# Kernel tuning notes

Hardware: AMD Instinct MI355X
Metric: run time of the kernel (lower is better)

## Reference

```python
import jax, jax.numpy as jnp
import numpy as np
from functools import partial

# norse LIFAdEx default parameters
DT = 0.001
TAU_SYN_INV = 1.0 / 5e-3   # 200.0
TAU_MEM_INV = 1.0 / 1e-2   # 100.0
TAU_ADA_INV = 2.0
ADAPT_CURRENT = 4.0
ADAPT_SPIKE = 0.02
DELTA_T = 0.5
V_LEAK = 0.0
V_TH = 1.0
V_RESET = 0.0
ALPHA = 100.0              # superspike surrogate sharpness
TAU_FILTER_INV = 223.1435511314


@jax.custom_vjp
def superspike(x):
    # forward: heaviside; backward: superspike surrogate grad
    return (x > 0).astype(x.dtype)

def _ss_fwd(x):
    return superspike(x), x

def _ss_bwd(x, g):
    return (g / (ALPHA * jnp.abs(x) + 1.0) ** 2,)

superspike.defvjp(_ss_fwd, _ss_bwd)


def lif_adex_recurrent(x, W_in, W_rec):
    """x: (T,B,F) -> spikes (T,B,H). norse lif_adex_step semantics."""
    T, B, _ = x.shape
    H = W_rec.shape[0]
    # precompute feed-forward input current for all steps: (T,B,H)
    i_in = jnp.einsum('tbf,hf->tbh', x, W_in)

    def step(carry, ic):
        z, v, i, a = carry
        dv = DT * TAU_MEM_INV * ((V_LEAK - v)
                                 + DELTA_T * jnp.exp((v - V_TH) / DELTA_T)
                                 + i - a)
        v_dec = v + dv
        i_dec = i - DT * TAU_SYN_INV * i
        a_dec = a + DT * TAU_ADA_INV * (ADAPT_CURRENT * (v - V_LEAK) - a)
        z_new = superspike(v_dec - V_TH)
        v_new = (1.0 - z_new) * v_dec + z_new * V_RESET
        i_new = i_dec + ic + z @ W_rec.T
        a_new = a_dec + z_new * ADAPT_SPIKE
        return (z_new, v_new, i_new, a_new), z_new

    z0 = jnp.zeros((B, H), x.dtype)
    init = (z0, z0, z0, z0)
    _, spikes = jax.lax.scan(step, init, i_in)
    return spikes


def exp_filter(spikes, W_out, b_out):
    """Linear readout + exponential low-pass filter over time."""
    y = jnp.einsum('tbh,oh->tbo', spikes, W_out) + b_out  # (T,B,O)
    k = DT * TAU_FILTER_INV

    def step(o_prev, y_t):
        o = o_prev + k * (y_t - o_prev)
        return o, o

    o0 = y[0]
    _, rest = jax.lax.scan(step, o0, y[1:])
    return jnp.concatenate([o0[None], rest], axis=0)


def setup_inputs() -> dict:
    key = jax.random.key(0)
    kx, k1, k2, k3, k4 = jax.random.split(key, 5)
    T, B, F, H, O = 500, 128, 128, 512, 32
    x = jax.random.normal(kx, (T, B, F), dtype=jnp.float32)
    W_in = jax.random.normal(k1, (H, F), dtype=jnp.float32) * np.sqrt(2.0 / F)
    W_rec = jax.random.normal(k2, (H, H), dtype=jnp.float32) * np.sqrt(2.0 / H)
    W_out = jax.random.normal(k3, (O, H), dtype=jnp.float32) * np.sqrt(1.0 / H)
    b_out = jax.random.normal(k4, (O,), dtype=jnp.float32) * 0.01
    return {'x': x, 'W_in': W_in, 'W_rec': W_rec, 'W_out': W_out, 'b_out': b_out}


def reference(x, W_in, W_rec, W_out, b_out):
    spikes = lif_adex_recurrent(x, W_in, W_rec)
    return exp_filter(spikes, W_out, b_out)
```

## Files before the change

### kernel.cpp

```cpp
#include <hip/hip_runtime.h>
#include <hip/hip_bf16.h>
#include <cstdint>
#include <cstddef>

#define T_STEPS 500
#define BATCH   128
#define FDIM    128
#define HDIM    512
#define ODIM    32
#define M_ROWS  (T_STEPS * BATCH)
#define ZOFF    (512u << 11)
#define ZOFFB   (512u << 10)

typedef __attribute__((ext_vector_type(8))) __bf16 bf16x8;
typedef __attribute__((ext_vector_type(4))) float  f32x4;

__device__ __forceinline__ float bfbits2f(unsigned short u) {
    union { unsigned int i; float f; } c; c.i = ((unsigned int)u) << 16; return c.f;
}
__device__ __forceinline__ float asf(unsigned int u) {
    union { unsigned int i; float f; } c; c.i = u; return c.f;
}
__device__ __forceinline__ void lds_barrier() {
    __builtin_amdgcn_sched_barrier(0);
    asm volatile("s_waitcnt lgkmcnt(0)" ::: "memory");
    __builtin_amdgcn_s_barrier();
    __builtin_amdgcn_sched_barrier(0);
}

__global__ void detect_kernel(const unsigned short* __restrict__ xw, int* __restrict__ flag) {
    __shared__ int cnt;
    if (threadIdx.x == 0) cnt = 0;
    __syncthreads();
    unsigned short w = xw[threadIdx.x * 2];
    int e = (w >> 7) & 0xFF;
    if (e >= 170) atomicAdd(&cnt, 1);
    __syncthreads();
    if (threadIdx.x == 0) *flag = (cnt >= 8) ? 1 : 0;
}

__global__ void prep_kernel(const void* __restrict__ Wrec,
                            const void* __restrict__ Wout,
                            const void* __restrict__ bout,
                            const void* __restrict__ Win,
                            const int* __restrict__ flag,
                            float* __restrict__ WrecT,
                            unsigned short* __restrict__ WrecTb,
                            float* __restrict__ WoutT,
                            float* __restrict__ WinT,
                            float* __restrict__ bout32) {
    const int fp32 = *flag;
    int idx = blockIdx.x * blockDim.x + threadIdx.x;
    if (fp32) {
        if (idx < HDIM * HDIM) {
            int h = idx / HDIM, hp = idx % HDIM;
            WrecT[hp * HDIM + h] = ((const float*)Wrec)[idx];
        }
        if (idx < HDIM) WrecT[HDIM * HDIM + idx] = 0.f;
        if (idx < HDIM * FDIM) {
            int h = idx / FDIM, f = idx % FDIM;
            WinT[f * HDIM + h] = ((const float*)Win)[idx];
        }
    } else {
        if (idx < HDIM * HDIM) {
            int h = idx / HDIM, hp = idx % HDIM;
            WrecTb[hp * HDIM + h] = ((const unsigned short*)Wrec)[idx];
        }
        if (idx < HDIM) WrecTb[HDIM * HDIM + idx] = 0;
    }
    if (idx < ODIM * HDIM) {
        int o = idx / HDIM, h = idx % HDIM;
        WoutT[h * ODIM + o] = fp32 ? ((const float*)Wout)[idx]
                                   : bfbits2f(((const unsigned short*)Wout)[idx]);
    }
    if (idx < ODIM)
        bout32[idx] = fp32 ? ((const float*)bout)[idx]
                           : bfbits2f(((const unsigned short*)bout)[idx]);
}

__global__ __launch_bounds__(256) void iin_gemm_mfma(const __hip_bfloat16* __restrict__ x,
                                                     const __hip_bfloat16* __restrict__ Win,
                                                     const int* __restrict__ flag,
                                                     float* __restrict__ iin) {
    if (*flag != 0) return;
    const int mt   = blockIdx.x;
    const int nt   = blockIdx.y;
    const int wave = threadIdx.x >> 6;
    const int lane = threadIdx.x & 63;
    const int l15  = lane & 15;
    const int quad = lane >> 4;
    const int m_base = mt * 64 + wave * 16;
    const int n_base = nt * 64;

    const __bf16* xb = reinterpret_cast<const __bf16*>(x);
    const __bf16* wb = reinterpret_cast<const __bf16*>(Win);

    f32x4 acc[4] = {{0.f,0.f,0.f,0.f},{0.f,0.f,0.f,0.f},{0.f,0.f,0.f,0.f},{0.f,0.f,0.f,0.f}};

#pragma unroll
    for (int kk = 0; kk < 4; ++kk) {
        const int k0 = kk * 32 + quad * 8;
        bf16x8 a = *reinterpret_cast<const bf16x8*>(xb + (size_t)(m_base + l15) * FDIM + k0);
#pragma unroll
        for (int nb = 0; nb < 4; ++nb) {
            bf16x8 bf = *reinterpret_cast<const bf16x8*>(wb + (size_t)(n_base + nb * 16 + l15) * FDIM + k0);
            acc[nb] = __builtin_amdgcn_mfma_f32_16x16x32_bf16(a, bf, acc[nb], 0, 0, 0);
        }
    }

#pragma unroll
    for (int nb = 0; nb < 4; ++nb)
#pragma unroll
        for (int r = 0; r < 4; ++r)
            iin[(size_t)(m_base + quad * 4 + r) * HDIM + n_base + nb * 16 + l15] = acc[nb][r];
}

__global__ __launch_bounds__(256) void iin_gemm_valu(const void* __restrict__ x,
                                                     const float* __restrict__ WinT,
                                                     const int* __restrict__ flag,
                                                     float* __restrict__ iin) {
    if (*flag != 1) return;
    const int tid = threadIdx.x;
    const int m0  = blockIdx.x * 32;
    const int tg  = tid >> 6;
    const int n0  = (tid & 63) * 8;

    __shared__ alignas(16) float xs[32][FDIM];

    for (int i = tid; i < 32 * FDIM; i += 256)
        xs[0][i] = ((const float*)x)[(size_t)m0 * FDIM + i];
    __syncthreads();

    const float4* xs4 = reinterpret_cast<const float4*>(&xs[tg * 8][0]);

    float acc[8][8];
#pragma unroll
    for (int i = 0; i < 8; ++i)
#pragma unroll
        for (int j = 0; j < 8; ++j) acc[i][j] = 0.f;

    auto ldw = [&](int k4, float (*w)[8]) {
#pragma unroll
        for (int u = 0; u < 4; ++u) {
            const float* wp = WinT + (size_t)(k4 * 4 + u) * HDIM + n0;
            float4 a = *(const float4*)(wp);
            float4 b = *(const float4*)(wp + 4);
            w[u][0] = a.x; w[u][1] = a.y; w[u][2] = a.z; w[u][3] = a.w;
            w[u][4] = b.x; w[u][5] = b.y; w[u][6] = b.z; w[u][7] = b.w;
        }
    };
    auto cmp = [&](int k4, const float (*w)[8]) {
#pragma unroll
        for (int i = 0; i < 8; ++i) {
            float4 xv = xs4[i * (FDIM / 4) + k4];
#pragma unroll
            for (int j = 0; j < 8; ++j)
                acc[i][j] += xv.x * w[0][j] + xv.y * w[1][j]
                           + xv.z * w[2][j] + xv.w * w[3][j];
        }
    };

    float wA[4][8], wB[4][8];
    ldw(0, wA);
    for (int k4 = 0; k4 < FDIM / 4; k4 += 2) {
        ldw(k4 + 1, wB);
        cmp(k4, wA);
        if (k4 + 2 < FDIM / 4) ldw(k4 + 2, wA);
        cmp(k4 + 1, wB);
    }

#pragma unroll
    for (int i = 0; i < 8; ++i) {
        float4 lo = {acc[i][0], acc[i][1], acc[i][2], acc[i][3]};
        float4 hi = {acc[i][4], acc[i][5], acc[i][6], acc[i][7]};
        float* op = iin + (size_t)(m0 + tg * 8 + i) * HDIM + n0;
        *(float4*)(op)     = lo;
        *(float4*)(op + 4) = hi;
    }
}

__global__ __launch_bounds__(1024) void scan_bf16(const float* __restrict__ iin,
                                                  const unsigned short* __restrict__ WrecTb,
                                                  const int* __restrict__ flag,
                                                  unsigned long long* __restrict__ masksG) {
    if (*flag != 0) return;
    const int b    = blockIdx.x;
    const int tid  = threadIdx.x;
    const int q    = tid & 63;
    const int pc   = tid >> 6;
    const int lane = tid & 63;
    const int wv   = tid >> 6;
    const bool st  = tid < HDIM;
    const int h    = tid;

    __shared__ unsigned long long wmask[8];
    __shared__ float4 partA[16][64];
    __shared__ float4 partB[16][64];
    __shared__ alignas(16) unsigned int slA[16][36];
    __shared__ alignas(16) unsigned int slB[16][36];
    unsigned int (*slO)[36] = slA;
    unsigned int (*slN)[36] = slB;

    float v = 0.f, cur = 0.f, a = 0.f;
    int   cnt = 0;
    const char* WQ = (const char*)WrecTb + q * 16;
    float ic_cur = st ? iin[(size_t)b * HDIM + h] : 0.f;

    for (int t = 0; t < T_STEPS; ++t) {
        float ic_next = 0.f;
        if (st && (t + 1) < T_STEPS)
            ic_next = iin[((size_t)(t + 1) * BATCH + b) * HDIM + h];

        float i_dec = 0.f; bool zk = false; unsigned long long m = 0;
        if (st) {
            float s = (0.0f - v) + 0.5f * expf((v - 1.0f) * 2.0f);
            s = s + cur;
            s = s - a;
            float v_dec = v + 0.1f * s;
            i_dec = cur - 0.2f * cur;
            float a_dec = a + 0.002f * (4.0f * v - a);
            zk = (v_dec - 1.0f) > 0.0f;
            m = __ballot(zk);
            if (lane == 0) {
                wmask[wv] = m;
                masksG[((size_t)t * BATCH + b) * 8 + wv] = m;
            }
            v = zk ? 0.0f : v_dec;
            a = zk ? (a_dec + 0.02f) : a_dec;
        }

        float rs0=0.f,rs1=0.f,rs2=0.f,rs3=0.f,rs4=0.f,rs5=0.f,rs6=0.f,rs7=0.f;
        {
            const unsigned int* sl = slO[pc];
            const int n  = (cnt + 15 - pc) >> 4;
            const int ng = (n + 3) >> 2;
            uint4 w0[4], w1[4];
            auto ldg = [&](int g, uint4* w) {
                uint4 ix = *(const uint4*)(sl + (g << 2));
                w[0] = *(const uint4*)(WQ + ix.x);
                w[1] = *(const uint4*)(WQ + ix.y);
                w[2] = *(const uint4*)(WQ + ix.z);
                w[3] = *(const uint4*)(WQ + ix.w);
            };
            auto accw = [&](const uint4* w) {
#pragma unroll
                for (int u = 0; u < 4; ++u) {
                    rs0 += asf(w[u].x << 16); rs1 += asf(w[u].x & 0xffff0000u);
                    rs2 += asf(w[u].y << 16); rs3 += asf(w[u].y & 0xffff0000u);
                    rs4 += asf(w[u].z << 16); rs5 += asf(w[u].z & 0xffff0000u);
                    rs6 += asf(w[u].w << 16); rs7 += asf(w[u].w & 0xffff0000u);
                }
            };
            int g = 0;
            if (ng > 0) ldg(0, w0);
            while (g + 2 <= ng) {
                ldg(g + 1, w1);
                accw(w0);
                if (g + 2 < ng) ldg(g + 2, w0);
                accw(w1);
                g += 2;
            }
            if (g < ng) accw(w0);
        }
        partA[pc][q] = (float4){rs0, rs1, rs2, rs3};
        partB[pc][q] = (float4){rs4, rs5, rs6, rs7};

        lds_barrier();

        int total = 0;
#pragma unroll
        for (int w = 0; w < 8; ++w) total += __popcll(wmask[w]);

        if (st) {
            float rec = 0.f;
            const int  qq = h >> 3, jj = h & 3;
            const bool hi = (h & 4) != 0;
#pragma unroll
            for (int pp = 0; pp < 16; ++pp) {
                const float* pa = (const float*)&partA[pp][qq];
                const float* pb = (const float*)&partB[pp][qq];
                rec += hi ? pb[jj] : pa[jj];
            }
            cur = (i_dec + ic_cur) + rec;

            if (zk) {
                int off = __popcll(m & ((1ull << lane) - 1ull));
#pragma unroll
                for (int w = 0; w < 8; ++w) if (w < wv) off += __popcll(wmask[w]);
                slN[off & 15][off >> 4] = (unsigned int)h << 10;
            }
        } else if (tid < HDIM + 64) {
            int s5 = (tid - HDIM) >> 2;
            int k  = (tid - HDIM) & 3;
            int ne = (total + 15 - s5) >> 4;
            int padc = (4 - (ne & 3)) & 3;
            if (k < padc) slN[s5][ne + k] = ZOFFB;
        }
        cnt = total;
        ic_cur = ic_next;

        lds_barrier();

        unsigned int (*tp)[36] = slO; slO = slN; slN = tp;
    }
}

__global__ __launch_bounds__(1024) void scan_f32(const float* __restrict__ iin,
                                                 const float* __restrict__ WrecT,
                                                 const int* __restrict__ flag,
                                                 unsigned long long* __restrict__ masksG) {
    if (*flag != 1) return;
    const int b    = blockIdx.x;
    const int tid  = threadIdx.x;
    const int lane = tid & 63;
    const int wv   = tid >> 6;
    const bool st  = tid < HDIM;
    const int h    = tid;
    const int p    = tid >> 7;
    const int q    = tid & 127;

    __shared__ alignas(16) unsigned int seg[2][8][64];
    __shared__ int scnt[2][8];
    __shared__ float4 part[2][8][128];

    if (tid < 8) scnt[1][tid] = 0;
    if (tid < 512) ((unsigned int*)seg[1])[tid] = ZOFF;
    lds_barrier();

    float v = 0.f, cur = 0.f, a = 0.f;
    const char* WQ = (const char*)WrecT + q * 16;

    for (int t = 0; t < T_STEPS; ++t) {
        const int cb = t & 1, pv = cb ^ 1;

        float ic = 0.f, i_dec = 0.f;
        if (st) {
            ic = iin[((size_t)t * BATCH + b) * HDIM + h];
            float s = (0.0f - v) + 0.5f * expf((v - 1.0f) * 2.0f);
            s = s + cur;
            s = s - a;
            float v_dec = v + 0.1f * s;
            i_dec = cur - 0.2f * cur;
            float a_dec = a + 0.002f * (4.0f * v - a);
            bool  zk = (v_dec - 1.0f) > 0.0f;
            unsigned long long m = __ballot(zk);
            int c = (int)__popcll(m);
            unsigned long long below = (1ull << lane) - 1ull;
            if (lane == 0) {
                scnt[cb][wv] = c;
                masksG[((size_t)t * BATCH + b) * 8 + wv] = m;
            }
            if (zk) {
                int off = (int)__popcll(m & below);
                seg[cb][wv][off] = (unsigned int)h << 11;
            } else {
                int pe = (c + 3) & ~3; pe = (pe < 4) ? 4 : pe;
                int ip = c + (int)__popcll(~m & below);
                if (ip < pe) seg[cb][wv][ip] = ZOFF;
            }
            v = zk ? 0.0f : v_dec;
            a = zk ? (a_dec + 0.02f) : a_dec;
        }

        {
            const int n  = scnt[pv][p];
            const int ng = (n + 3) >> 2;
            const unsigned int* sp = &seg[pv][p][0];
            float4 rs = {0.f, 0.f, 0.f, 0.f};
            float4 b0[4], b1[4];
            auto ld4 = [&](int g, float4* d) {
                uint4 i0 = *(const uint4*)(sp + (g << 2));
                d[0] = *(const float4*)(WQ + i0.x);
                d[1] = *(const float4*)(WQ + i0.y);
                d[2] = *(const float4*)(WQ + i0.z);
                d[3] = *(const float4*)(WQ + i0.w);
            };
            auto acc4 = [&](const float4* d) {
#pragma unroll
                for (int u = 0; u < 4; ++u) {
                    rs.x += d[u].x; rs.y += d[u].y; rs.z += d[u].z; rs.w += d[u].w;
                }
            };
            ld4(0, b0);
            int g = 0;
            while (g + 2 <= ng) {
                ld4(g + 1, b1);
                acc4(b0);
                if (g + 2 < ng) ld4(g + 2, b0);
                acc4(b1);
                g += 2;
            }
            if (g < ng) acc4(b0);
            part[cb][p][q] = rs;
        }

        lds_barrier();

        if (st) {
            float rec = 0.f;
#pragma unroll
            for (int pp = 0; pp < 8; ++pp)
                rec += ((const float*)&part[cb][pp][h >> 2])[h & 3];
            cur = (i_dec + ic) + rec;
        }
    }
}

__global__ __launch_bounds__(256) void y_kernel(const unsigned long long* __restrict__ masks,
                                                const float* __restrict__ WoutT,
                                                const float* __restrict__ bout,
                                                float* __restrict__ y) {
    const int tid = threadIdx.x;
    const int p   = blockIdx.x * 8 + (tid >> 5);
    const int o   = tid & 31;
    const unsigned long long* mp = masks + (size_t)p * 8;
    float acc = 0.f;
#pragma unroll
    for (int w = 0; w < 8; ++w) {
        unsigned long long m = mp[w];
        const float* Wb = WoutT + (size_t)w * 64 * ODIM + o;
        while (m) {
            int j = __builtin_ctzll(m);
            acc += Wb[j * ODIM];
            m &= m - 1;
        }
    }
    y[(size_t)p * ODIM + o] = acc + bout[o];
}

__global__ __launch_bounds__(64) void filter_kernel(const float* __restrict__ y,
                                                    const int* __restrict__ flag,
                                                    void* __restrict__ out) {
    const int p = blockIdx.x * 64 + threadIdx.x;
    const int fp32o = *flag;
    const float kf = 0.2231435511314f;
    float c0[10], c1[10];
#pragma unroll
    for (int u = 0; u < 10; ++u) c0[u] = y[(size_t)u * (BATCH * ODIM) + p];
    float o_state = 0.f;
    for (int base = 0; base < T_STEPS; base += 10) {
        if (base + 10 < T_STEPS) {
#pragma unroll
            for (int u = 0; u < 10; ++u)
                c1[u] = y[(size_t)(base + 10 + u) * (BATCH * ODIM) + p];
        }
#pragma unroll
        for (int u = 0; u < 10; ++u) {
            int t = base + u;
            float yt = c0[u];
            o_state = (t == 0) ? yt : (o_state + kf * (yt - o_state));
            size_t oi = (size_t)t * (BATCH * ODIM) + p;
            if (fp32o) ((float*)out)[oi] = o_state;
            else       ((__hip_bfloat16*)out)[oi] = __float2bfloat16(o_state);
        }
#pragma unroll
        for (int u = 0; u < 10; ++u) c0[u] = c1[u];
    }
}

extern "C" void kernel_launch(void* const* d_in, const int* in_sizes, int n_in,
                              void* d_out, int out_size, void* d_ws, size_t ws_size,
                              hipStream_t stream) {
    const void* x = d_in[0]; const void* Win = d_in[1]; const void* Wrec = d_in[2];
    const void* Wout = d_in[3]; const void* bout = d_in[4];
    for (int i = 0; i < n_in; ++i) {
        switch (in_sizes[i]) {
            case 8192000: x    = d_in[i]; break;
            case 65536:   Win  = d_in[i]; break;
            case 262144:  Wrec = d_in[i]; break;
            case 16384:   Wout = d_in[i]; break;
            case 32:      bout = d_in[i]; break;
            default: break;
        }
    }

    const size_t OFF_FLAG  = 0;
    const size_t OFF_BOUT  = 256;
    const size_t OFF_WOUTT = 512;
    const size_t OFF_WRECT = 66048;
    const size_t OFF_WINT  = 1116672;
    const size_t OFF_MASK  = 1378816;
    const size_t OFF_IIN   = 5474816;
    const size_t OFF_Y     = OFF_IIN;
    const size_t REQUIRED  = OFF_IIN + (size_t)M_ROWS * HDIM * 4;
    if (ws_size < REQUIRED) return;

    char* ws = (char*)d_ws;
    int*            flag   = (int*)(ws + OFF_FLAG);
    float*          bout32 = (float*)(ws + OFF_BOUT);
    float*          WoutT  = (float*)(ws + OFF_WOUTT);
    float*          WrecT  = (float*)(ws + OFF_WRECT);
    unsigned short* WrecTb = (unsigned short*)(ws + OFF_WRECT);
    float*          WinT   = (float*)(ws + OFF_WINT);
    unsigned long long* masks = (unsigned long long*)(ws + OFF_MASK);
    float*          iin    = (float*)(ws + OFF_IIN);
    float*          y      = (float*)(ws + OFF_Y);

    hipLaunchKernelGGL(detect_kernel, dim3(1), dim3(256), 0, stream,
                       (const unsigned short*)x, flag);
    hipLaunchKernelGGL(prep_kernel, dim3((HDIM * HDIM + 255) / 256), dim3(256), 0, stream,
                       Wrec, Wout, bout, Win, flag, WrecT, WrecTb, WoutT, WinT, bout32);
    hipLaunchKernelGGL(iin_gemm_mfma, dim3(M_ROWS / 64, HDIM / 64), dim3(256), 0, stream,
                       (const __hip_bfloat16*)x, (const __hip_bfloat16*)Win, flag, iin);
    hipLaunchKernelGGL(iin_gemm_valu, dim3(M_ROWS / 32), dim3(256), 0, stream,
                       x, WinT, flag, iin);
    hipLaunchKernelGGL(scan_bf16, dim3(BATCH), dim3(1024), 0, stream,
                       iin, WrecTb, flag, masks);
    hipLaunchKernelGGL(scan_f32, dim3(BATCH), dim3(1024), 0, stream,
                       iin, WrecT, flag, masks);
    hipLaunchKernelGGL(y_kernel, dim3(M_ROWS / 8), dim3(256), 0, stream,
                       masks, WoutT, bout32, y);
    hipLaunchKernelGGL(filter_kernel, dim3((BATCH * ODIM) / 64), dim3(64), 0, stream,
                       y, flag, d_out);
}
```

Baseline: 819.6 us.

## Split scan block into state and gather wavefronts, pipelining recurrent sum across steps

The scan kernel now gives threads 0-511 the neuron-state update and threads 512-1023 the sparse recurrent gather, so the two run concurrently within a step. Each gather thread covers 8 output columns (two float4 loads per spike) instead of 4, and it writes separate A/B partial buffers. The reduction of partials moves to the start of the next step's state update, which removes one barrier per step. The cost is more registers per gather thread and a one-step skew in bookkeeping (ic_prev/i_dec_prev) that must stay numerically equivalent.

```diff
diff --git a/kernel.cpp b/kernel.cpp
--- a/kernel.cpp
+++ b/kernel.cpp
@@ -316,31 +316,51 @@
     const int wv   = tid >> 6;
     const bool st  = tid < HDIM;
     const int h    = tid;
-    const int p    = tid >> 7;
-    const int q    = tid & 127;
 
     __shared__ alignas(16) unsigned int seg[2][8][64];
     __shared__ int scnt[2][8];
-    __shared__ float4 part[2][8][128];
+    __shared__ float4 partA[2][8][64];
+    __shared__ float4 partB[2][8][64];
 
     if (tid < 8) scnt[1][tid] = 0;
-    if (tid < 512) ((unsigned int*)seg[1])[tid] = ZOFF;
+    if (tid < 512) {
+        ((unsigned int*)seg[1])[tid] = ZOFF;
+        ((float4*)partA[1])[tid] = (float4){0.f, 0.f, 0.f, 0.f};
+        ((float4*)partB[1])[tid] = (float4){0.f, 0.f, 0.f, 0.f};
+    }
     lds_barrier();
 
-    float v = 0.f, cur = 0.f, a = 0.f;
-    const char* WQ = (const char*)WrecT + q * 16;
+    float v = 0.f, a = 0.f;
+    float i_dec_prev = 0.f;
+    float ic_prev = 0.f;
+
+    const int gt = tid - 512;
+    const int p  = (gt >> 6) & 7;
+    const int j  = gt & 63;
+    const char* WQ8 = (const char*)WrecT + j * 32;
 
     for (int t = 0; t < T_STEPS; ++t) {
         const int cb = t & 1, pv = cb ^ 1;
 
-        float ic = 0.f, i_dec = 0.f;
         if (st) {
-            ic = iin[((size_t)t * BATCH + b) * HDIM + h];
+            float rec = 0.f;
+            const int  jj = h >> 3, kk = h & 3;
+            const bool hi = (h & 4) != 0;
+#pragma unroll
+            for (int pp = 0; pp < 8; ++pp) {
+                const float* pa = (const float*)&partA[pv][pp][jj];
+                const float* pb = (const float*)&partB[pv][pp][jj];
+                rec += hi ? pb[kk] : pa[kk];
+            }
+            float cur = (i_dec_prev + ic_prev) + rec;
+
+            float ic_t = iin[((size_t)t * BATCH + b) * HDIM + h];
+
             float s = (0.0f - v) + 0.5f * expf((v - 1.0f) * 2.0f);
             s = s + cur;
             s = s - a;
             float v_dec = v + 0.1f * s;
-            i_dec = cur - 0.2f * cur;
+            i_dec_prev = cur - 0.2f * cur;
             float a_dec = a + 0.002f * (4.0f * v - a);
             bool  zk = (v_dec - 1.0f) > 0.0f;
             unsigned long long m = __ballot(zk);
@@ -360,49 +380,48 @@
             }
             v = zk ? 0.0f : v_dec;
             a = zk ? (a_dec + 0.02f) : a_dec;
-        }
-
-        {
+            ic_prev = ic_t;
+        } else {
             const int n  = scnt[pv][p];
             const int ng = (n + 3) >> 2;
             const unsigned int* sp = &seg[pv][p][0];
-            float4 rs = {0.f, 0.f, 0.f, 0.f};
-            float4 b0[4], b1[4];
-            auto ld4 = [&](int g, float4* d) {
-                uint4 i0 = *(const uint4*)(sp + (g << 2));
-                d[0] = *(const float4*)(WQ + i0.x);
-                d[1] = *(const float4*)(WQ + i0.y);
-                d[2] = *(const float4*)(WQ + i0.z);
-                d[3] = *(const float4*)(WQ + i0.w);
+            float rs0=0.f,rs1=0.f,rs2=0.f,rs3=0.f,rs4=0.f,rs5=0.f,rs6=0.f,rs7=0.f;
+            float4 w0[8], w1[8];
+            auto ldg = [&](int g, float4* w) {
+                uint4 ix = *(const uint4*)(sp + (g << 2));
+                w[0] = *(const float4*)(WQ8 + ix.x);
+                w[1] = *(const float4*)(WQ8 + ix.x + 16);
+                w[2] = *(const float4*)(WQ8 + ix.y);
+                w[3] = *(const float4*)(WQ8 + ix.y + 16);
+                w[4] = *(const float4*)(WQ8 + ix.z);
+                w[5] = *(const float4*)(WQ8 + ix.z + 16);
+                w[6] = *(const float4*)(WQ8 + ix.w);
+                w[7] = *(const float4*)(WQ8 + ix.w + 16);
             };
-            auto acc4 = [&](const float4* d) {
+            auto accw = [&](const float4* w) {
 #pragma unroll
                 for (int u = 0; u < 4; ++u) {
-                    rs.x += d[u].x; rs.y += d[u].y; rs.z += d[u].z; rs.w += d[u].w;
+                    rs0 += w[2*u].x;   rs1 += w[2*u].y;
+                    rs2 += w[2*u].z;   rs3 += w[2*u].w;
+                    rs4 += w[2*u+1].x; rs5 += w[2*u+1].y;
+                    rs6 += w[2*u+1].z; rs7 += w[2*u+1].w;
                 }
             };
-            ld4(0, b0);
+            ldg(0, w0);
             int g = 0;
             while (g + 2 <= ng) {
-                ld4(g + 1, b1);
-                acc4(b0);
-                if (g + 2 < ng) ld4(g + 2, b0);
-                acc4(b1);
+                ldg(g + 1, w1);
+                accw(w0);
+                if (g + 2 < ng) ldg(g + 2, w0);
+                accw(w1);
                 g += 2;
             }
-            if (g < ng) acc4(b0);
-            part[cb][p][q] = rs;
+            if (g < ng) accw(w0);
+            partA[cb][p][j] = (float4){rs0, rs1, rs2, rs3};
+            partB[cb][p][j] = (float4){rs4, rs5, rs6, rs7};
         }
 
         lds_barrier();
-
-        if (st) {
-            float rec = 0.f;
-#pragma unroll
-            for (int pp = 0; pp < 8; ++pp)
-                rec += ((const float*)&part[cb][pp][h >> 2])[h & 3];
-            cur = (i_dec + ic) + rec;
-        }
     }
 }
 
```

New measurement: 841.5 us. 1.03x slower.

## Restructure f32 scan so each thread sums its own recurrent column, one barrier

Applied to the files above, without the earlier changes.

The f32 recurrent scan now runs 512 threads per batch, each owning one hidden unit. Each thread gathers the W_rec^T entries for the previous step's spike list directly, instead of eight partitions computing float4 partial sums that are then reduced through shared memory. This removes the partial-sum array and the second barrier per time step. The first 8 spike indices of every wave segment are padded to 8 with the zero-row offset and loaded unconditionally, so those weight loads are issued before the neuron update. Longer segments go through a tail loop. The trade-off is more scalar loads per thread instead of float4 loads, and fewer threads to spread that work over.

```diff
diff --git a/kernel.cpp b/kernel.cpp
--- a/kernel.cpp
+++ b/kernel.cpp
@@ -305,104 +305,109 @@
     }
 }
 
-__global__ __launch_bounds__(1024) void scan_f32(const float* __restrict__ iin,
-                                                 const float* __restrict__ WrecT,
-                                                 const int* __restrict__ flag,
-                                                 unsigned long long* __restrict__ masksG) {
+__global__ __launch_bounds__(512, 2) void scan_f32(const float* __restrict__ iin,
+                                                   const float* __restrict__ WrecT,
+                                                   const int* __restrict__ flag,
+                                                   unsigned long long* __restrict__ masksG) {
     if (*flag != 1) return;
     const int b    = blockIdx.x;
     const int tid  = threadIdx.x;
     const int lane = tid & 63;
     const int wv   = tid >> 6;
-    const bool st  = tid < HDIM;
     const int h    = tid;
-    const int p    = tid >> 7;
-    const int q    = tid & 127;
 
     __shared__ alignas(16) unsigned int seg[2][8][64];
-    __shared__ int scnt[2][8];
-    __shared__ float4 part[2][8][128];
+    __shared__ alignas(16) int scnt[2][8];
 
     if (tid < 8) scnt[1][tid] = 0;
-    if (tid < 512) ((unsigned int*)seg[1])[tid] = ZOFF;
+    ((unsigned int*)seg[1])[tid] = ZOFF;
     lds_barrier();
 
     float v = 0.f, cur = 0.f, a = 0.f;
-    const char* WQ = (const char*)WrecT + q * 16;
+    const char* Wc = (const char*)WrecT + (size_t)h * 4;
 
     for (int t = 0; t < T_STEPS; ++t) {
         const int cb = t & 1, pv = cb ^ 1;
 
-        float ic = 0.f, i_dec = 0.f;
-        if (st) {
-            ic = iin[((size_t)t * BATCH + b) * HDIM + h];
-            float s = (0.0f - v) + 0.5f * expf((v - 1.0f) * 2.0f);
-            s = s + cur;
-            s = s - a;
-            float v_dec = v + 0.1f * s;
-            i_dec = cur - 0.2f * cur;
-            float a_dec = a + 0.002f * (4.0f * v - a);
-            bool  zk = (v_dec - 1.0f) > 0.0f;
-            unsigned long long m = __ballot(zk);
-            int c = (int)__popcll(m);
-            unsigned long long below = (1ull << lane) - 1ull;
-            if (lane == 0) {
-                scnt[cb][wv] = c;
-                masksG[((size_t)t * BATCH + b) * 8 + wv] = m;
-            }
-            if (zk) {
-                int off = (int)__popcll(m & below);
-                seg[cb][wv][off] = (unsigned int)h << 11;
-            } else {
-                int pe = (c + 3) & ~3; pe = (pe < 4) ? 4 : pe;
-                int ip = c + (int)__popcll(~m & below);
-                if (ip < pe) seg[cb][wv][ip] = ZOFF;
-            }
-            v = zk ? 0.0f : v_dec;
-            a = zk ? (a_dec + 0.02f) : a_dec;
-        }
+        const uint4 scA = *(const uint4*)&scnt[pv][0];
+        const uint4 scB = *(const uint4*)&scnt[pv][4];
+        uint4 s0[8], s1[8];
+#pragma unroll
+        for (int s = 0; s < 8; ++s) {
+            s0[s] = *(const uint4*)&seg[pv][s][0];
+            s1[s] = *(const uint4*)&seg[pv][s][4];
+        }
+        float w[8][8];
+#pragma unroll
+        for (int s = 0; s < 8; ++s) {
+            w[s][0] = *(const float*)(Wc + s0[s].x);
+            w[s][1] = *(const float*)(Wc + s0[s].y);
+            w[s][2] = *(const float*)(Wc + s0[s].z);
+            w[s][3] = *(const float*)(Wc + s0[s].w);
+            w[s][4] = *(const float*)(Wc + s1[s].x);
+            w[s][5] = *(const float*)(Wc + s1[s].y);
+            w[s][6] = *(const float*)(Wc + s1[s].z);
+            w[s][7] = *(const float*)(Wc + s1[s].w);
+        }
+
+        float ic = iin[((size_t)t * BATCH + b) * HDIM + h];
+
+        float s_ = (0.0f - v) + 0.5f * expf((v - 1.0f) * 2.0f);
+        s_ = s_ + cur;
+        s_ = s_ - a;
+        float v_dec = v + 0.1f * s_;
+        float i_dec = cur - 0.2f * cur;
+        float a_dec = a + 0.002f * (4.0f * v - a);
+        bool  zk = (v_dec - 1.0f) > 0.0f;
+        unsigned long long m = __ballot(zk);
+        int c = (int)__popcll(m);
+        unsigned long long below = (1ull << lane) - 1ull;
+        if (lane == 0) {
+            scnt[cb][wv] = c;
+            masksG[((size_t)t * BATCH + b) * 8 + wv] = m;
+        }
+        if (zk) {
+            int off = (int)__popcll(m & below);
+            seg[cb][wv][off] = (unsigned int)h << 11;
+        } else {
+            int pe = (c + 7) & ~7; if (pe < 8) pe = 8;
+            int ip = c + (int)__popcll(~m & below);
+            if (ip < pe) seg[cb][wv][ip] = ZOFF;
+        }
+        v = zk ? 0.0f : v_dec;
+        a = zk ? (a_dec + 0.02f) : a_dec;
+
+        float rec = 0.f;
+#pragma unroll
+        for (int s = 0; s < 8; ++s)
+#pragma unroll
+            for (int k = 0; k < 8; ++k)
+                rec += w[s][k];
 
         {
-            const int n  = scnt[pv][p];
-            const int ng = (n + 3) >> 2;
-            const unsigned int* sp = &seg[pv][p][0];
-            float4 rs = {0.f, 0.f, 0.f, 0.f};
-            float4 b0[4], b1[4];
-            auto ld4 = [&](int g, float4* d) {
-                uint4 i0 = *(const uint4*)(sp + (g << 2));
-                d[0] = *(const float4*)(WQ + i0.x);
-                d[1] = *(const float4*)(WQ + i0.y);
-                d[2] = *(const float4*)(WQ + i0.z);
-                d[3] = *(const float4*)(WQ + i0.w);
-            };
-            auto acc4 = [&](const float4* d) {
-#pragma unroll
-                for (int u = 0; u < 4; ++u) {
-                    rs.x += d[u].x; rs.y += d[u].y; rs.z += d[u].z; rs.w += d[u].w;
+            auto tail = [&](int s, int cs) {
+                int pe = (cs + 7) & ~7;
+                for (int e = 8; e < pe; e += 4) {
+                    uint4 ix = *(const uint4*)&seg[pv][s][e];
+                    rec += *(const float*)(Wc + ix.x);
+                    rec += *(const float*)(Wc + ix.y);
+                    rec += *(const float*)(Wc + ix.z);
+                    rec += *(const float*)(Wc + ix.w);
                 }
             };
-            ld4(0, b0);
-            int g = 0;
-            while (g + 2 <= ng) {
-                ld4(g + 1, b1);
-                acc4(b0);
-                if (g + 2 < ng) ld4(g + 2, b0);
-                acc4(b1);
-                g += 2;
-            }
-            if (g < ng) acc4(b0);
-            part[cb][p][q] = rs;
-        }
+            if (scA.x > 8) tail(0, scA.x);
+            if (scA.y > 8) tail(1, scA.y);
+            if (scA.z > 8) tail(2, scA.z);
+            if (scA.w > 8) tail(3, scA.w);
+            if (scB.x > 8) tail(4, scB.x);
+            if (scB.y > 8) tail(5, scB.y);
+            if (scB.z > 8) tail(6, scB.z);
+            if (scB.w > 8) tail(7, scB.w);
+        }
+
+        cur = (i_dec + ic) + rec;
 
         lds_barrier();
-
-        if (st) {
-            float rec = 0.f;
-#pragma unroll
-            for (int pp = 0; pp < 8; ++pp)
-                rec += ((const float*)&part[cb][pp][h >> 2])[h & 3];
-            cur = (i_dec + ic) + rec;
-        }
     }
 }
 
@@ -506,7 +511,7 @@
                        x, WinT, flag, iin);
     hipLaunchKernelGGL(scan_bf16, dim3(BATCH), dim3(1024), 0, stream,
                        iin, WrecTb, flag, masks);
-    hipLaunchKernelGGL(scan_f32, dim3(BATCH), dim3(1024), 0, stream,
+    hipLaunchKernelGGL(scan_f32, dim3(BATCH), dim3(512), 0, stream,
                        iin, WrecT, flag, masks);
     hipLaunchKernelGGL(y_kernel, dim3(M_ROWS / 8), dim3(256), 0, stream,
                        masks, WoutT, bout32, y);
```

Result: slower. 1.111 ms (+35.5%).
